# Performance work log

Measured on AMD Instinct MI355X. Metric: run time of the kernel, lower is better.

## Reference

```python
import jax, jax.numpy as jnp
import numpy as np

D_TOK = 1222
N_BOU = 80

def _pe(n, d):
    pos = np.arange(n, dtype=np.float32)[:, None]
    div = np.exp(np.arange(0, d, 2, dtype=np.float32) * (-np.log(10000.0) / d))
    pe = np.zeros((n, d), np.float32)
    pe[:, 0::2] = np.sin(pos * div)
    pe[:, 1::2] = np.cos(pos * div)
    return jnp.asarray(pe)

def _ln(x, g, b, eps=1e-5):
    m = jnp.mean(x, -1, keepdims=True)
    v = jnp.mean((x - m) ** 2, -1, keepdims=True)
    return (x - m) / jnp.sqrt(v + eps) * g + b

_gather = jax.vmap(lambda f, i: f[:, i[..., 0], i[..., 1]])  # f [C,H,W], i [...,2] -> [C,...]


def setup_inputs() -> dict:
    key = jax.random.key(0)
    ks = jax.random.split(key, 8)
    D, FF, N = D_TOK, 2048, N_BOU
    s = 0.02
    return {
        "curr_img_features": jax.random.normal(ks[0], (2, 1024, 224, 224), jnp.float32),
        "previous_boundary": jax.random.randint(ks[1], (2, N, 2), 0, 224, dtype=jnp.int32),
        "ln_g": jnp.ones((D,), jnp.float32), "ln_b": jnp.zeros((D,), jnp.float32),
        "in_proj_w": s * jax.random.normal(ks[2], (3 * D, D), jnp.float32),
        "in_proj_b": jnp.zeros((3 * D,), jnp.float32),
        "out_proj_w": s * jax.random.normal(ks[3], (D, D), jnp.float32),
        "out_proj_b": jnp.zeros((D,), jnp.float32),
        "lin1_w": s * jax.random.normal(ks[4], (FF, D), jnp.float32),
        "lin1_b": jnp.zeros((FF,), jnp.float32),
        "lin2_w": s * jax.random.normal(ks[5], (D, FF), jnp.float32),
        "lin2_b": jnp.zeros((D,), jnp.float32),
        "norm1_g": jnp.ones((D,), jnp.float32), "norm1_b": jnp.zeros((D,), jnp.float32),
        "norm2_g": jnp.ones((D,), jnp.float32), "norm2_b": jnp.zeros((D,), jnp.float32),
        "fc_w": s * jax.random.normal(ks[6], (N, 1026, D), jnp.float32),
        "fc_b": jnp.zeros((N, 1026), jnp.float32),
    }


def reference(curr_img_features, previous_boundary, ln_g, ln_b, in_proj_w, in_proj_b,
              out_proj_w, out_proj_b, lin1_w, lin1_b, lin2_w, lin2_b,
              norm1_g, norm1_b, norm2_g, norm2_b, fc_w, fc_b):
    D = D_TOK
    offs = jnp.array([[dx, dy] for dx in range(-3, 4) for dy in range(-3, 4)], jnp.int32)  # [49,2]
    # multi-scale avg-pooled + zero-padded maps (hoisted out of the refine loop; identical math)
    padded = []
    for s in range(4):
        k = 2 ** s
        f = curr_img_features
        if k > 1:
            B, C, H, W = f.shape
            f = f.reshape(B, C, H // k, k, W // k, k).mean((3, 5))
        padded.append(jnp.pad(f, ((0, 0), (0, 0), (3, 3), (3, 3))))
    pe = _pe(N_BOU, D)
    boundary = previous_boundary.astype(jnp.int32)
    results = []
    for _ in range(6):
        qf = _gather(curr_img_features, boundary)  # [B,C,N]
        dots = []
        for s in range(4):
            bs = boundary // (2 ** s)
            idx = bs[:, :, None, :] + offs[None, None] + 3  # [B,N,49,2] into padded map
            keyf = _gather(padded[s], idx)  # [B,C,N,49]
            dots.append(jnp.einsum('bcn,bcno->bno', qf, keyf))
        dots = jnp.concatenate(dots, axis=2)  # [B,N,196]
        tokens = jnp.concatenate([qf.transpose(0, 2, 1), dots,
                                  boundary.astype(jnp.float32)], axis=2)  # [B,N,1222]
        tokens = _ln(tokens, ln_g, ln_b)
        tokens = tokens + pe[None]  # positional encoding (dropout = eval/identity)
        # TransformerEncoderLayer, nhead=1, post-norm, relu, no dropout (eval)
        qkv = tokens @ in_proj_w.T + in_proj_b
        q, k_, v = jnp.split(qkv, 3, axis=-1)
        sc = jnp.einsum('bnd,bmd->bnm', q, k_) / jnp.sqrt(jnp.float32(D))
        attn = jax.nn.softmax(sc, axis=-1) @ v
        attn = attn @ out_proj_w.T + out_proj_b
        x = _ln(tokens + attn, norm1_g, norm1_b)
        ff = jax.nn.relu(x @ lin1_w.T + lin1_b) @ lin2_w.T + lin2_b
        x = _ln(x + ff, norm2_g, norm2_b)
        # 80 independent per-token heads, batched
        out = jnp.einsum('bnd,nod->bno', x, fc_w) + fc_b[None]  # [B,80,1026]
        off_f = out[..., :2]
        # torch .long() truncates toward zero; clip keeps gathers in-range (original clamp was a no-op bug)
        boundary = jnp.clip(boundary + jnp.trunc(off_f).astype(jnp.int32), 0, 223)
        results.append(boundary)
    return jnp.stack(results)  # [6,B,80,2] int32
```

## Files before the change

### kernel.cpp

```cpp
#include <hip/hip_runtime.h>
#include <math.h>

#define DTOK 1222
#define NBOU 80
#define MM   160
#define FFD  2048
#define OQKV 3666

typedef __attribute__((ext_vector_type(8))) short short8;
typedef __attribute__((ext_vector_type(4))) float f32x4;

__device__ __forceinline__ unsigned short f2bf(float x) {
  unsigned int u = __float_as_uint(x);
  unsigned int r = (u + 0x7FFFu + ((u >> 16) & 1u)) >> 16;
  return (unsigned short)r;
}
__device__ __forceinline__ float bf2f(unsigned short h) {
  return __uint_as_float((unsigned int)h << 16);
}

__device__ __forceinline__ float wave_red_sum(float v) {
#pragma unroll
  for (int off = 32; off; off >>= 1) v += __shfl_xor(v, off, 64);
  return v;
}
__device__ __forceinline__ float block_red_sum(float v, float* rb, int tid) {
  v = wave_red_sum(v);
  __syncthreads();
  if ((tid & 63) == 0) rb[tid >> 6] = v;
  __syncthreads();
  return rb[0] + rb[1] + rb[2] + rb[3];
}

__device__ __forceinline__ void frag_write_row(const float* __restrict__ row,
                                               short* __restrict__ Af,
                                               int r, int T, int tid) {
  int mt = r >> 6, mf = (r >> 4) & 3, rl = r & 15;
  for (int task = tid; task < T * 4; task += 256) {
    int t = task >> 2, kq = task & 3;
    const float* src = row + t * 32 + kq * 8;
    short8 h, l, q;
#pragma unroll
    for (int j = 0; j < 8; ++j) {
      float x = src[j];
      unsigned short hb = f2bf(x);
      float r1 = x - bf2f(hb);
      unsigned short lb = f2bf(r1);
      float r2 = r1 - bf2f(lb);
      h[j] = (short)hb; l[j] = (short)lb; q[j] = (short)f2bf(r2);
    }
    size_t base = (size_t)(mt * T + t) * 6144 + mf * 512 + (size_t)(rl + kq * 16) * 8;
    *(short8*)(Af + base) = h;
    *(short8*)(Af + base + 2048) = l;
    *(short8*)(Af + base + 4096) = q;
  }
}

__global__ __launch_bounds__(256) void k_nhwc0p(const float* __restrict__ f,
                                                float* __restrict__ L0n,
                                                float* __restrict__ L1) {
  int xt = blockIdx.x;
  int y1 = blockIdx.y;
  int zc = blockIdx.z;
  int b = zc >> 4, ct = zc & 15;
  __shared__ float tile[64][65];
  int tid = threadIdx.x;
  const float* fb = f + (size_t)b * 1024 * 50176;
#pragma unroll
  for (int i = 0; i < 16; ++i) {
    int u = tid + 256 * i;
    int xl = u & 31, r = (u >> 5) & 1, c = u >> 6;
    tile[c][xl + 32 * r] = fb[(size_t)(ct * 64 + c) * 50176 +
                              (size_t)(2 * y1 + r) * 224 + xt * 32 + xl];
  }
  __syncthreads();
#pragma unroll
  for (int i = 0; i < 16; ++i) {
    int u = tid + 256 * i;
    int c2 = u & 63, x2 = (u >> 6) & 31, r2 = u >> 11;
    L0n[(((size_t)b * 224 + 2 * y1 + r2) * 224 + xt * 32 + x2) * 1024 + ct * 64 + c2] =
        tile[c2][x2 + 32 * r2];
  }
#pragma unroll
  for (int i = 0; i < 4; ++i) {
    int u = tid + 256 * i;
    int c3 = u & 63, xp = u >> 6;
    float v = 0.25f * (tile[c3][2 * xp] + tile[c3][2 * xp + 1] +
                       tile[c3][32 + 2 * xp] + tile[c3][32 + 2 * xp + 1]);
    L1[(((size_t)b * 112 + y1) * 112 + xt * 16 + xp) * 1024 + ct * 64 + c3] = v;
  }
}

__global__ __launch_bounds__(256) void k_pool23(const float* __restrict__ L1,
                                                float* __restrict__ L2,
                                                float* __restrict__ L3) {
  int x3 = blockIdx.x, y3 = blockIdx.y, b = blockIdx.z;
  int c = threadIdx.x * 4;
  float4 l2v[2][2];
#pragma unroll
  for (int yy = 0; yy < 2; ++yy)
#pragma unroll
    for (int xx = 0; xx < 2; ++xx) {
      const float* p00 = L1 + (((size_t)(b * 112 + 4 * y3 + 2 * yy) * 112) + 4 * x3 + 2 * xx) * 1024 + c;
      const float* p01 = p00 + 1024;
      const float* p10 = p00 + (size_t)112 * 1024;
      const float* p11 = p10 + 1024;
      float4 a = *(const float4*)p00, bv = *(const float4*)p01;
      float4 cv = *(const float4*)p10, dv = *(const float4*)p11;
      float4 r;
      r.x = 0.25f * (a.x + bv.x + cv.x + dv.x);
      r.y = 0.25f * (a.y + bv.y + cv.y + dv.y);
      r.z = 0.25f * (a.z + bv.z + cv.z + dv.z);
      r.w = 0.25f * (a.w + bv.w + cv.w + dv.w);
      l2v[yy][xx] = r;
      *(float4*)(L2 + (((size_t)(b * 56 + 2 * y3 + yy) * 56) + 2 * x3 + xx) * 1024 + c) = r;
    }
  float4 r3;
  r3.x = 0.25f * (l2v[0][0].x + l2v[0][1].x + l2v[1][0].x + l2v[1][1].x);
  r3.y = 0.25f * (l2v[0][0].y + l2v[0][1].y + l2v[1][0].y + l2v[1][1].y);
  r3.z = 0.25f * (l2v[0][0].z + l2v[0][1].z + l2v[1][0].z + l2v[1][1].z);
  r3.w = 0.25f * (l2v[0][0].w + l2v[0][1].w + l2v[1][0].w + l2v[1][1].w);
  *(float4*)(L3 + (((size_t)(b * 28 + y3) * 28) + x3) * 1024 + c) = r3;
}

__global__ __launch_bounds__(256) void k_pe(float* __restrict__ pe, int* __restrict__ bnd,
                                            const int* __restrict__ pb) {
  int n = blockIdx.x, tid = threadIdx.x;
  for (int d = tid; d < DTOK; d += 256) {
    int i = d >> 1;
    double e = exp((double)(2 * i) * (-log(10000.0) / (double)DTOK));
    double ang = (double)n * e;
    pe[n * DTOK + d] = (float)((d & 1) ? cos(ang) : sin(ang));
  }
  if (n == 0) {
    for (int t = tid; t < 2 * NBOU * 2; t += 256) bnd[t] = pb[t];
  }
}

__global__ __launch_bounds__(256) void k_conv(const float* __restrict__ X,
                                              short* __restrict__ F,
                                              int R, int K, int T) {
  int b = blockIdx.x;
  int rt = b / T, t = b % T;
  int tid = threadIdx.x, mf = tid >> 6, lane = tid & 63;
  int row = rt * 64 + mf * 16 + (lane & 15);
  int k0 = t * 32 + (lane >> 4) * 8;
  float a[8];
#pragma unroll
  for (int j = 0; j < 8; ++j) {
    int k = k0 + j;
    a[j] = (row < R && k < K) ? X[(size_t)row * K + k] : 0.f;
  }
  short8 h, l, q;
#pragma unroll
  for (int j = 0; j < 8; ++j) {
    float x = a[j];
    unsigned short hb = f2bf(x);
    float r1 = x - bf2f(hb);
    unsigned short lb = f2bf(r1);
    float r2 = r1 - bf2f(lb);
    h[j] = (short)hb; l[j] = (short)lb; q[j] = (short)f2bf(r2);
  }
  size_t base = (size_t)b * 6144 + mf * 512 + (size_t)lane * 8;
  *(short8*)(F + base) = h;
  *(short8*)(F + base + 2048) = l;
  *(short8*)(F + base + 4096) = q;
}

__global__ __launch_bounds__(256) void k_dots(const float* __restrict__ L0n,
                                              const float* __restrict__ L1,
                                              const float* __restrict__ L2,
                                              const float* __restrict__ L3,
                                              const int* __restrict__ bnd,
                                              float* __restrict__ dots) {
  int o = blockIdx.x;
  int blk = blockIdx.y;
  int b = blk / NBOU;
  int tid = threadIdx.x, s = tid >> 6, lane = tid & 63;
  int bd0 = bnd[blk * 2 + 0], bd1 = bnd[blk * 2 + 1];
  const float* cp = L0n + (((size_t)b * 224 + bd0) * 224 + bd1) * 1024;
  int Hs = 224 >> s;
  const float* base = (s == 0) ? L0n : (s == 1) ? L1 : (s == 2) ? L2 : L3;
  int yy = (bd0 >> s) + o / 7 - 3;
  int xx = (bd1 >> s) + o % 7 - 3;
  float a = 0.f;
  if (yy >= 0 && yy < Hs && xx >= 0 && xx < Hs) {
    const float* kp = base + (((size_t)b * Hs + yy) * Hs + xx) * 1024;
#pragma unroll
    for (int j = 0; j < 4; ++j) {
      int c = (lane + 64 * j) * 4;
      float4 kv = *(const float4*)(kp + c);
      float4 qv = *(const float4*)(cp + c);
      a += kv.x * qv.x + kv.y * qv.y + kv.z * qv.z + kv.w * qv.w;
    }
  }
  a = wave_red_sum(a);
  if (lane == 0) dots[blk * 196 + s * 49 + o] = a;
}

__global__ __launch_bounds__(256) void k_tokln(const float* __restrict__ L0n,
                                               const int* __restrict__ bnd,
                                               const float* __restrict__ dots,
                                               const float* __restrict__ g,
                                               const float* __restrict__ bb,
                                               const float* __restrict__ pe,
                                               float* __restrict__ tok_out,
                                               short* __restrict__ Af, int T) {
  int blk = blockIdx.x;
  int b = blk / NBOU, n = blk % NBOU;
  int tid = threadIdx.x;
  __shared__ __align__(16) float token[1248];
  __shared__ float rbuf[8];
  int bd0 = bnd[blk * 2 + 0], bd1 = bnd[blk * 2 + 1];
  const float* cp = L0n + (((size_t)b * 224 + bd0) * 224 + bd1) * 1024;
  {
    int d = tid * 4;
    *(float4*)&token[d] = *(const float4*)(cp + d);
  }
  if (tid < 196) token[1024 + tid] = dots[blk * 196 + tid];
  if (tid == 0) { token[1220] = (float)bd0; token[1221] = (float)bd1; }
  if (tid < 26) token[1222 + tid] = 0.f;
  __syncthreads();

  float ls = 0.f;
  for (int d = tid; d < DTOK; d += 256) ls += token[d];
  float mean = block_red_sum(ls, rbuf, tid) * (1.0f / DTOK);
  float lq = 0.f;
  for (int d = tid; d < DTOK; d += 256) { float t = token[d] - mean; lq += t * t; }
  float var = block_red_sum(lq, rbuf, tid) * (1.0f / DTOK);
  float rstd = rsqrtf(var + 1e-5f);
  for (int d = tid; d < DTOK; d += 256) {
    float o = (token[d] - mean) * rstd * g[d] + bb[d] + pe[n * DTOK + d];
    tok_out[(size_t)blk * DTOK + d] = o;
    token[d] = o;
  }
  __syncthreads();
  frag_write_row(token, Af, blk, T, tid);
}

__global__ __launch_bounds__(256) void k_mfma2(const short* __restrict__ Af,
                                               const short* __restrict__ Bf,
                                               float* __restrict__ partial,
                                               int T, int O, int S) {
  int nt = blockIdx.x, sp = blockIdx.y;
  int tid = threadIdx.x, w = tid >> 6, lane = tid & 63;
  int wr = w >> 1, wc = w & 1;
  int rl = lane & 15, kq = lane >> 4;
  int cps = (T + S - 1) / S;
  int t0 = sp * cps, t1 = min(t0 + cps, T);

  f32x4 acc[3][2][2];
#pragma unroll
  for (int mt = 0; mt < 3; ++mt)
#pragma unroll
    for (int mi = 0; mi < 2; ++mi)
#pragma unroll
      for (int ni = 0; ni < 2; ++ni) acc[mt][mi][ni] = (f32x4){0.f, 0.f, 0.f, 0.f};

  const size_t bbase = (size_t)(wc * 2) * 512 + (size_t)lane * 8;
  const size_t abase = (size_t)(wr * 2) * 512 + (size_t)lane * 8;

  short8 bv[3][2], bv2[3][2];

#define LOADB(tt, BV)                                                          \
  {                                                                            \
    const short* bp = Bf + ((size_t)nt * T + (tt)) * 6144 + bbase;             \
    _Pragma("unroll")                                                          \
    for (int s = 0; s < 3; ++s)                                                \
      _Pragma("unroll")                                                        \
      for (int ni = 0; ni < 2; ++ni)                                           \
        BV[s][ni] = *(const short8*)(bp + s * 2048 + ni * 512);                \
  }

  if (t0 < t1) {
    LOADB(t0, bv);
    for (int t = t0; t < t1; ++t) {
      if (t + 1 < t1) LOADB(t + 1, bv2);
#pragma unroll
      for (int mt = 0; mt < 3; ++mt) {
        const short* ap = Af + ((size_t)(mt * T + t)) * 6144 + abase;
        short8 af[3][2];
#pragma unroll
        for (int s = 0; s < 3; ++s)
#pragma unroll
          for (int mi = 0; mi < 2; ++mi)
            af[s][mi] = *(const short8*)(ap + s * 2048 + mi * 512);
#pragma unroll
        for (int mi = 0; mi < 2; ++mi)
#pragma unroll
          for (int ni = 0; ni < 2; ++ni) {
            f32x4 a = acc[mt][mi][ni];
            a = __builtin_amdgcn_mfma_f32_16x16x32_bf16(af[0][mi], bv[0][ni], a, 0, 0, 0);
            a = __builtin_amdgcn_mfma_f32_16x16x32_bf16(af[0][mi], bv[1][ni], a, 0, 0, 0);
            a = __builtin_amdgcn_mfma_f32_16x16x32_bf16(af[1][mi], bv[0][ni], a, 0, 0, 0);
            a = __builtin_amdgcn_mfma_f32_16x16x32_bf16(af[0][mi], bv[2][ni], a, 0, 0, 0);
            a = __builtin_amdgcn_mfma_f32_16x16x32_bf16(af[2][mi], bv[0][ni], a, 0, 0, 0);
            a = __builtin_amdgcn_mfma_f32_16x16x32_bf16(af[1][mi], bv[1][ni], a, 0, 0, 0);
            acc[mt][mi][ni] = a;
          }
      }
#pragma unroll
      for (int s = 0; s < 3; ++s)
#pragma unroll
        for (int ni = 0; ni < 2; ++ni) bv[s][ni] = bv2[s][ni];
    }
  }
#undef LOADB

  float* pp = partial + (size_t)sp * MM * O;
#pragma unroll
  for (int mt = 0; mt < 3; ++mt)
#pragma unroll
    for (int mi = 0; mi < 2; ++mi)
#pragma unroll
      for (int ni = 0; ni < 2; ++ni) {
        int c = nt * 64 + wc * 32 + ni * 16 + rl;
        if (c >= O) continue;
#pragma unroll
        for (int reg = 0; reg < 4; ++reg) {
          int r = mt * 64 + wr * 32 + mi * 16 + kq * 4 + reg;
          if (r < MM) pp[(size_t)r * O + c] = acc[mt][mi][ni][reg];
        }
      }
}

__global__ __launch_bounds__(256) void k_red4(const float* __restrict__ partial,
                                              const float* __restrict__ bias,
                                              float* __restrict__ out,
                                              int O, int S) {
  size_t idx = ((size_t)blockIdx.x * 256 + threadIdx.x) * 4;
  size_t total = (size_t)MM * O;
  if (idx >= total) return;
  float4 v = *(const float4*)(partial + idx);
  for (int s = 1; s < S; ++s) {
    float4 p = *(const float4*)(partial + (size_t)s * total + idx);
    v.x += p.x; v.y += p.y; v.z += p.z; v.w += p.w;
  }
  float r[4] = {v.x, v.y, v.z, v.w};
#pragma unroll
  for (int j = 0; j < 4; ++j) r[j] += bias[(int)((idx + j) % O)];
  float4 wv = {r[0], r[1], r[2], r[3]};
  *(float4*)(out + idx) = wv;
}

__global__ __launch_bounds__(256) void k_redf(const float* __restrict__ partial,
                                              const float* __restrict__ bias,
                                              short* __restrict__ Af,
                                              int S, int T) {
  const int O = FFD;
  size_t idx8 = ((size_t)blockIdx.x * 256 + threadIdx.x) * 8;
  size_t total = (size_t)MM * O;
  if (idx8 >= total) return;
  int r = (int)(idx8 / O), c = (int)(idx8 % O);
  float v[8];
#pragma unroll
  for (int j = 0; j < 8; ++j) v[j] = 0.f;
  for (int s = 0; s < S; ++s) {
    const float* p = partial + (size_t)s * total + idx8;
#pragma unroll
    for (int j = 0; j < 8; ++j) v[j] += p[j];
  }
  short8 h, l, q;
#pragma unroll
  for (int j = 0; j < 8; ++j) {
    float x = fmaxf(v[j] + bias[c + j], 0.f);
    unsigned short hb = f2bf(x);
    float r1 = x - bf2f(hb);
    unsigned short lb = f2bf(r1);
    float r2 = r1 - bf2f(lb);
    h[j] = (short)hb; l[j] = (short)lb; q[j] = (short)f2bf(r2);
  }
  int mt = r >> 6, mf = (r >> 4) & 3, rl = r & 15;
  int t = c >> 5, kq = (c >> 3) & 3;
  size_t base = (size_t)(mt * T + t) * 6144 + mf * 512 + (size_t)(rl + kq * 16) * 8;
  *(short8*)(Af + base) = h;
  *(short8*)(Af + base + 2048) = l;
  *(short8*)(Af + base + 4096) = q;
}

__global__ __launch_bounds__(256) void k_redln(const float* __restrict__ partial,
                                               const float* __restrict__ bias,
                                               const float* __restrict__ res,
                                               const float* __restrict__ g,
                                               const float* __restrict__ bb,
                                               float* __restrict__ xout,
                                               short* __restrict__ Af,
                                               int S, int T) {
  const int O = DTOK;
  int m = blockIdx.x, tid = threadIdx.x;
  __shared__ __align__(16) float row[1248];
  __shared__ float rb[8];
  if (tid < 26) row[1222 + tid] = 0.f;
  float ls = 0.f;
  for (int d = tid; d < O; d += 256) {
    float v = 0.f;
    for (int s = 0; s < S; ++s) v += partial[((size_t)s * MM + m) * O + d];
    v += bias[d];
    v += res[(size_t)m * O + d];
    row[d] = v; ls += v;
  }
  float mean = block_red_sum(ls, rb, tid) * (1.0f / DTOK);
  float lq = 0.f;
  for (int d = tid; d < O; d += 256) { float t = row[d] - mean; lq += t * t; }
  float var = block_red_sum(lq, rb, tid) * (1.0f / DTOK);
  float rstd = rsqrtf(var + 1e-5f);
  for (int d = tid; d < O; d += 256) {
    float xn = (row[d] - mean) * rstd * g[d] + bb[d];
    xout[(size_t)m * O + d] = xn;
    row[d] = xn;
  }
  __syncthreads();
  frag_write_row(row, Af, m, T, tid);
}

__global__ __launch_bounds__(256) void k_redlnfc(const float* __restrict__ partial,
                                                 const float* __restrict__ bias,
                                                 const float* __restrict__ res,
                                                 const float* __restrict__ g,
                                                 const float* __restrict__ bb,
                                                 const float* __restrict__ fcw,
                                                 const float* __restrict__ fcb,
                                                 int* __restrict__ bnd,
                                                 int* __restrict__ outp,
                                                 int S) {
  const int O = DTOK;
  int blk = blockIdx.x;
  int n = blk % NBOU;
  int tid = threadIdx.x;
  __shared__ float row[DTOK];
  __shared__ float rb[8];
  float ls = 0.f;
  for (int d = tid; d < O; d += 256) {
    float v = 0.f;
    for (int s = 0; s < S; ++s) v += partial[((size_t)s * MM + blk) * O + d];
    v += bias[d];
    v += res[(size_t)blk * O + d];
    row[d] = v; ls += v;
  }
  float mean = block_red_sum(ls, rb, tid) * (1.0f / DTOK);
  float lq = 0.f;
  for (int d = tid; d < O; d += 256) { float t = row[d] - mean; lq += t * t; }
  float var = block_red_sum(lq, rb, tid) * (1.0f / DTOK);
  float rstd = rsqrtf(var + 1e-5f);
  const float* w0 = fcw + (size_t)n * 1026 * DTOK;
  const float* w1 = w0 + DTOK;
  float s0 = 0.f, s1 = 0.f;
  for (int d = tid; d < O; d += 256) {
    float xn = (row[d] - mean) * rstd * g[d] + bb[d];
    s0 += xn * w0[d];
    s1 += xn * w1[d];
  }
  s0 = block_red_sum(s0, rb, tid);
  s1 = block_red_sum(s1, rb, tid);
  if (tid == 0) {
    float o0 = s0 + fcb[n * 1026 + 0];
    float o1 = s1 + fcb[n * 1026 + 1];
    int b0 = bnd[blk * 2 + 0], b1 = bnd[blk * 2 + 1];
    int nb0 = b0 + (int)truncf(o0);
    int nb1 = b1 + (int)truncf(o1);
    nb0 = nb0 < 0 ? 0 : (nb0 > 223 ? 223 : nb0);
    nb1 = nb1 < 0 ? 0 : (nb1 > 223 ? 223 : nb1);
    bnd[blk * 2 + 0] = nb0;
    bnd[blk * 2 + 1] = nb1;
    outp[blk * 2 + 0] = nb0;
    outp[blk * 2 + 1] = nb1;
  }
}

__global__ __launch_bounds__(512) void k_attn3(const float* __restrict__ qkv,
                                               short* __restrict__ Af, int T) {
  int blk = blockIdx.x;
  int b = blk / NBOU;
  int tid = threadIdx.x, w = tid >> 6, lane = tid & 63;
  __shared__ __align__(16) float q[1224];
  __shared__ float sc[80];
  __shared__ __align__(16) float pv[8][1248];
  const float* qrow = qkv + (size_t)blk * OQKV;
  for (int d = tid; d < DTOK; d += 512) q[d] = qrow[d];
  __syncthreads();

#pragma unroll
  for (int i = 0; i < 10; ++i) {
    int m2 = w * 10 + i;
    const float* krow = qkv + (size_t)(b * NBOU + m2) * OQKV + DTOK;
    float a = 0.f;
#pragma unroll
    for (int j = 0; j < 20; ++j) {
      int d = lane + 64 * j;
      if (d < DTOK) a += q[d] * krow[d];
    }
    a = wave_red_sum(a);
    if (lane == 0) sc[m2] = a * (1.0f / 34.957116f);
  }
  __syncthreads();
  if (w == 0) {
    float x0 = sc[lane];
    float x1 = (lane < 16) ? sc[64 + lane] : -INFINITY;
    float mx = fmaxf(x0, x1);
#pragma unroll
    for (int off = 32; off; off >>= 1) mx = fmaxf(mx, __shfl_xor(mx, off, 64));
    float e0 = expf(x0 - mx);
    float e1 = (lane < 16) ? expf(x1 - mx) : 0.f;
    float ssum = wave_red_sum(e0 + e1);
    sc[lane] = e0 / ssum;
    if (lane < 16) sc[64 + lane] = e1 / ssum;
  }
  __syncthreads();

  float acc[20];
#pragma unroll
  for (int j = 0; j < 20; ++j) acc[j] = 0.f;
  for (int i = 0; i < 10; ++i) {
    int m2 = w * 10 + i;
    float pm = sc[m2];
    const float* vrow = qkv + (size_t)(b * NBOU + m2) * OQKV + 2 * DTOK;
#pragma unroll
    for (int j = 0; j < 20; ++j) {
      int d = lane + 64 * j;
      if (d < DTOK) acc[j] += pm * vrow[d];
    }
  }
#pragma unroll
  for (int j = 0; j < 20; ++j) {
    int d = lane + 64 * j;
    if (d < DTOK) pv[w][d] = acc[j];
  }
  __syncthreads();
  for (int d = tid; d < DTOK; d += 512) {
    float v = pv[0][d];
#pragma unroll
    for (int s = 1; s < 8; ++s) v += pv[s][d];
    pv[0][d] = v;
  }
  if (tid < 26) pv[0][1222 + tid] = 0.f;
  __syncthreads();
  frag_write_row(pv[0], Af, blk, T, tid);
}

extern "C" void kernel_launch(void* const* d_in, const int* in_sizes, int n_in,
                              void* d_out, int out_size, void* d_ws, size_t ws_size,
                              hipStream_t stream) {
  const float* f   = (const float*)d_in[0];
  const int*   pb  = (const int*)d_in[1];
  const float* lng = (const float*)d_in[2];
  const float* lnb = (const float*)d_in[3];
  const float* ipw = (const float*)d_in[4];
  const float* ipb = (const float*)d_in[5];
  const float* opw = (const float*)d_in[6];
  const float* opb = (const float*)d_in[7];
  const float* l1w = (const float*)d_in[8];
  const float* l1b = (const float*)d_in[9];
  const float* l2w = (const float*)d_in[10];
  const float* l2b = (const float*)d_in[11];
  const float* n1g = (const float*)d_in[12];
  const float* n1b = (const float*)d_in[13];
  const float* n2g = (const float*)d_in[14];
  const float* n2b = (const float*)d_in[15];
  const float* fcw = (const float*)d_in[16];
  const float* fcb = (const float*)d_in[17];
  int* outp = (int*)d_out;

  const int T1 = 39;
  const int T2 = 64;
  const int NT_IP = 58, NT_OP = 20, NT_L1 = 32, NT_L2 = 20;
  const int S_IP = 6, S_OP = 10, S_L1 = 8, S_L2 = 16;

  char* wsb = (char*)d_ws;
  auto alloc = [&](size_t bytes) -> char* {
    char* p = wsb;
    wsb += (bytes + 255) & ~(size_t)255;
    return p;
  };
  float* L0n  = (float*)alloc((size_t)2 * 224 * 224 * 1024 * 4);
  float* L1   = (float*)alloc((size_t)2 * 112 * 112 * 1024 * 4);
  float* L2   = (float*)alloc((size_t)2 * 56 * 56 * 1024 * 4);
  float* L3   = (float*)alloc((size_t)2 * 28 * 28 * 1024 * 4);
  float* pe   = (float*)alloc((size_t)NBOU * DTOK * 4);
  int*   bnd  = (int*)alloc(320 * 4);
  float* tokens = (float*)alloc((size_t)MM * DTOK * 4);
  float* qkvb   = (float*)alloc((size_t)MM * OQKV * 4);
  float* x1     = (float*)alloc((size_t)MM * DTOK * 4);
  float* dots   = (float*)alloc((size_t)MM * 196 * 4);
  short* Af1  = (short*)alloc((size_t)3 * T1 * 6144 * 2);
  short* Af2  = (short*)alloc((size_t)3 * T2 * 6144 * 2);
  short* ipWf = (short*)alloc((size_t)NT_IP * T1 * 6144 * 2);
  short* opWf = (short*)alloc((size_t)NT_OP * T1 * 6144 * 2);
  short* l1Wf = (short*)alloc((size_t)NT_L1 * T1 * 6144 * 2);
  short* l2Wf = (short*)alloc((size_t)NT_L2 * T2 * 6144 * 2);
  float* part = (float*)alloc((size_t)S_IP * MM * OQKV * 4);

  k_nhwc0p<<<dim3(7, 112, 32), 256, 0, stream>>>(f, L0n, L1);
  k_pool23<<<dim3(28, 28, 2), 256, 0, stream>>>(L1, L2, L3);
  k_pe<<<NBOU, 256, 0, stream>>>(pe, bnd, pb);

  k_conv<<<NT_IP * T1, 256, 0, stream>>>(ipw, ipWf, OQKV, DTOK, T1);
  k_conv<<<NT_OP * T1, 256, 0, stream>>>(opw, opWf, DTOK, DTOK, T1);
  k_conv<<<NT_L1 * T1, 256, 0, stream>>>(l1w, l1Wf, FFD, DTOK, T1);
  k_conv<<<NT_L2 * T2, 256, 0, stream>>>(l2w, l2Wf, DTOK, FFD, T2);

  for (int it = 0; it < 6; ++it) {
    k_dots<<<dim3(49, 160), 256, 0, stream>>>(L0n, L1, L2, L3, bnd, dots);
    k_tokln<<<160, 256, 0, stream>>>(L0n, bnd, dots, lng, lnb, pe, tokens, Af1, T1);

    k_mfma2<<<dim3(NT_IP, S_IP), 256, 0, stream>>>(Af1, ipWf, part, T1, OQKV, S_IP);
    k_red4<<<(MM * OQKV + 1023) / 1024, 256, 0, stream>>>(part, ipb, qkvb, OQKV, S_IP);

    k_attn3<<<160, 512, 0, stream>>>(qkvb, Af1, T1);

    k_mfma2<<<dim3(NT_OP, S_OP), 256, 0, stream>>>(Af1, opWf, part, T1, DTOK, S_OP);
    k_redln<<<160, 256, 0, stream>>>(part, opb, tokens, n1g, n1b, x1, Af1, S_OP, T1);

    k_mfma2<<<dim3(NT_L1, S_L1), 256, 0, stream>>>(Af1, l1Wf, part, T1, FFD, S_L1);
    k_redf<<<MM * FFD / 2048, 256, 0, stream>>>(part, l1b, Af2, S_L1, T2);

    k_mfma2<<<dim3(NT_L2, S_L2), 256, 0, stream>>>(Af2, l2Wf, part, T2, DTOK, S_L2);
    k_redlnfc<<<160, 256, 0, stream>>>(part, l2b, x1, n2g, n2b, fcw, fcb, bnd, outp + it * 320, S_L2);
  }
}
```

Measured before the change: 1.269 ms.

## Fuse refine-loop kernels into one persistent cooperative kernel with grid syncs

Replaces the 66 per-iteration kernel launches (dots, token LN, four split-K GEMMs, reductions, attention, LN/fc head) with a single cooperative persistent kernel. It loops over the phases with grid-wide barriers and grid-stride task loops, and falls back to separate launches if the cooperative launch fails. Attention is also rewritten to run with 256 threads (4 waves) instead of 512. The aim is to remove launch overhead and inter-kernel gaps in a latency-bound loop. The cost is grid.sync overhead, fewer resident blocks (2 per CU under launch bounds), and some phases running with less parallelism than before.

New measurement: 4.037 ms. +218.2%, slower.

```diff
diff --git a/kernel.cpp b/kernel.cpp
--- a/kernel.cpp
+++ b/kernel.cpp
@@ -1,11 +1,25 @@
 #include <hip/hip_runtime.h>
+#include <hip/hip_cooperative_groups.h>
 #include <math.h>
+
+namespace cg = cooperative_groups;
 
 #define DTOK 1222
 #define NBOU 80
 #define MM   160
 #define FFD  2048
 #define OQKV 3666
+
+#define T1c 39
+#define T2c 64
+#define NT_IPc 58
+#define NT_OPc 20
+#define NT_L1c 32
+#define NT_L2c 20
+#define S_IPc 6
+#define S_OPc 10
+#define S_L1c 8
+#define S_L2c 16
 
 typedef __attribute__((ext_vector_type(8))) short short8;
 typedef __attribute__((ext_vector_type(4))) float f32x4;
@@ -59,9 +73,7 @@
 __global__ __launch_bounds__(256) void k_nhwc0p(const float* __restrict__ f,
                                                 float* __restrict__ L0n,
                                                 float* __restrict__ L1) {
-  int xt = blockIdx.x;
-  int y1 = blockIdx.y;
-  int zc = blockIdx.z;
+  int xt = blockIdx.x, y1 = blockIdx.y, zc = blockIdx.z;
   int b = zc >> 4, ct = zc & 15;
   __shared__ float tile[64][65];
   int tid = threadIdx.x;
@@ -167,374 +179,412 @@
   *(short8*)(F + base + 4096) = q;
 }
 
-__global__ __launch_bounds__(256) void k_dots(const float* __restrict__ L0n,
-                                              const float* __restrict__ L1,
-                                              const float* __restrict__ L2,
-                                              const float* __restrict__ L3,
-                                              const int* __restrict__ bnd,
-                                              float* __restrict__ dots) {
-  int o = blockIdx.x;
-  int blk = blockIdx.y;
-  int b = blk / NBOU;
-  int tid = threadIdx.x, s = tid >> 6, lane = tid & 63;
-  int bd0 = bnd[blk * 2 + 0], bd1 = bnd[blk * 2 + 1];
-  const float* cp = L0n + (((size_t)b * 224 + bd0) * 224 + bd1) * 1024;
-  int Hs = 224 >> s;
-  const float* base = (s == 0) ? L0n : (s == 1) ? L1 : (s == 2) ? L2 : L3;
-  int yy = (bd0 >> s) + o / 7 - 3;
-  int xx = (bd1 >> s) + o % 7 - 3;
-  float a = 0.f;
-  if (yy >= 0 && yy < Hs && xx >= 0 && xx < Hs) {
-    const float* kp = base + (((size_t)b * Hs + yy) * Hs + xx) * 1024;
-#pragma unroll
-    for (int j = 0; j < 4; ++j) {
-      int c = (lane + 64 * j) * 4;
-      float4 kv = *(const float4*)(kp + c);
-      float4 qv = *(const float4*)(cp + c);
-      a += kv.x * qv.x + kv.y * qv.y + kv.z * qv.z + kv.w * qv.w;
-    }
-  }
-  a = wave_red_sum(a);
-  if (lane == 0) dots[blk * 196 + s * 49 + o] = a;
-}
-
-__global__ __launch_bounds__(256) void k_tokln(const float* __restrict__ L0n,
-                                               const int* __restrict__ bnd,
-                                               const float* __restrict__ dots,
-                                               const float* __restrict__ g,
-                                               const float* __restrict__ bb,
-                                               const float* __restrict__ pe,
-                                               float* __restrict__ tok_out,
-                                               short* __restrict__ Af, int T) {
-  int blk = blockIdx.x;
-  int b = blk / NBOU, n = blk % NBOU;
+struct Params {
+  const float *L0n, *L1, *L2, *L3;
+  const float *lng, *lnb, *pe;
+  const float *ipb, *opb, *l1b, *l2b;
+  const float *n1g, *n1b, *n2g, *n2b;
+  const float *fcw, *fcb;
+  const short *ipWf, *opWf, *l1Wf, *l2Wf;
+  short *Af1, *Af2;
+  float *tokens, *qkvb, *x1, *dots, *part;
+  int *bnd, *outp;
+};
+
+__device__ __forceinline__ void ph_dots(const Params& p, int tid) {
+  int s = tid >> 6, lane = tid & 63;
+  for (int task = blockIdx.x; task < 49 * 160; task += gridDim.x) {
+    int o = task % 49, blk = task / 49;
+    int b = blk / NBOU;
+    int bd0 = p.bnd[blk * 2 + 0], bd1 = p.bnd[blk * 2 + 1];
+    const float* cp = p.L0n + (((size_t)b * 224 + bd0) * 224 + bd1) * 1024;
+    int Hs = 224 >> s;
+    const float* base = (s == 0) ? p.L0n : (s == 1) ? p.L1 : (s == 2) ? p.L2 : p.L3;
+    int yy = (bd0 >> s) + o / 7 - 3;
+    int xx = (bd1 >> s) + o % 7 - 3;
+    float a = 0.f;
+    if (yy >= 0 && yy < Hs && xx >= 0 && xx < Hs) {
+      const float* kp = base + (((size_t)b * Hs + yy) * Hs + xx) * 1024;
+#pragma unroll
+      for (int j = 0; j < 4; ++j) {
+        int c = (lane + 64 * j) * 4;
+        float4 kv = *(const float4*)(kp + c);
+        float4 qv = *(const float4*)(cp + c);
+        a += kv.x * qv.x + kv.y * qv.y + kv.z * qv.z + kv.w * qv.w;
+      }
+    }
+    a = wave_red_sum(a);
+    if (lane == 0) p.dots[blk * 196 + s * 49 + o] = a;
+  }
+}
+
+__device__ __forceinline__ void ph_tokln(const Params& p, int tid,
+                                         float* token, float* rbuf) {
+  for (int blk = blockIdx.x; blk < 160; blk += gridDim.x) {
+    int b = blk / NBOU, n = blk % NBOU;
+    int bd0 = p.bnd[blk * 2 + 0], bd1 = p.bnd[blk * 2 + 1];
+    const float* cp = p.L0n + (((size_t)b * 224 + bd0) * 224 + bd1) * 1024;
+    {
+      int d = tid * 4;
+      *(float4*)&token[d] = *(const float4*)(cp + d);
+    }
+    if (tid < 196) token[1024 + tid] = p.dots[blk * 196 + tid];
+    if (tid == 0) { token[1220] = (float)bd0; token[1221] = (float)bd1; }
+    if (tid < 26) token[1222 + tid] = 0.f;
+    __syncthreads();
+    float ls = 0.f;
+    for (int d = tid; d < DTOK; d += 256) ls += token[d];
+    float mean = block_red_sum(ls, rbuf, tid) * (1.0f / DTOK);
+    float lq = 0.f;
+    for (int d = tid; d < DTOK; d += 256) { float t = token[d] - mean; lq += t * t; }
+    float var = block_red_sum(lq, rbuf, tid) * (1.0f / DTOK);
+    float rstd = rsqrtf(var + 1e-5f);
+    for (int d = tid; d < DTOK; d += 256) {
+      float o = (token[d] - mean) * rstd * p.lng[d] + p.lnb[d] + p.pe[n * DTOK + d];
+      p.tokens[(size_t)blk * DTOK + d] = o;
+      token[d] = o;
+    }
+    __syncthreads();
+    frag_write_row(token, p.Af1, blk, T1c, tid);
+    __syncthreads();
+  }
+}
+
+__device__ __forceinline__ void ph_gemm(const short* __restrict__ Af,
+                                        const short* __restrict__ Bf,
+                                        float* __restrict__ partial,
+                                        int T, int O, int S, int NT, int tid) {
+  int w = tid >> 6, lane = tid & 63;
+  int wr = w >> 1, wc = w & 1;
+  int rl = lane & 15, kq = lane >> 4;
+  const size_t bbase = (size_t)(wc * 2) * 512 + (size_t)lane * 8;
+  const size_t abase = (size_t)(wr * 2) * 512 + (size_t)lane * 8;
+  for (int task = blockIdx.x; task < NT * S; task += gridDim.x) {
+    int nt = task % NT, sp = task / NT;
+    int cps = (T + S - 1) / S;
+    int t0 = sp * cps, t1 = min(t0 + cps, T);
+    f32x4 acc[3][2][2];
+#pragma unroll
+    for (int mt = 0; mt < 3; ++mt)
+#pragma unroll
+      for (int mi = 0; mi < 2; ++mi)
+#pragma unroll
+        for (int ni = 0; ni < 2; ++ni) acc[mt][mi][ni] = (f32x4){0.f, 0.f, 0.f, 0.f};
+    short8 bv[3][2], bv2[3][2];
+#define LOADB(tt, BV)                                                          \
+    {                                                                          \
+      const short* bp = Bf + ((size_t)nt * T + (tt)) * 6144 + bbase;           \
+      _Pragma("unroll")                                                        \
+      for (int s = 0; s < 3; ++s)                                              \
+        _Pragma("unroll")                                                      \
+        for (int ni = 0; ni < 2; ++ni)                                         \
+          BV[s][ni] = *(const short8*)(bp + s * 2048 + ni * 512);              \
+    }
+    if (t0 < t1) {
+      LOADB(t0, bv);
+      for (int t = t0; t < t1; ++t) {
+        if (t + 1 < t1) LOADB(t + 1, bv2);
+#pragma unroll
+        for (int mt = 0; mt < 3; ++mt) {
+          const short* ap = Af + ((size_t)(mt * T + t)) * 6144 + abase;
+          short8 af[3][2];
+#pragma unroll
+          for (int s = 0; s < 3; ++s)
+#pragma unroll
+            for (int mi = 0; mi < 2; ++mi)
+              af[s][mi] = *(const short8*)(ap + s * 2048 + mi * 512);
+#pragma unroll
+          for (int mi = 0; mi < 2; ++mi)
+#pragma unroll
+            for (int ni = 0; ni < 2; ++ni) {
+              f32x4 a = acc[mt][mi][ni];
+              a = __builtin_amdgcn_mfma_f32_16x16x32_bf16(af[0][mi], bv[0][ni], a, 0, 0, 0);
+              a = __builtin_amdgcn_mfma_f32_16x16x32_bf16(af[0][mi], bv[1][ni], a, 0, 0, 0);
+              a = __builtin_amdgcn_mfma_f32_16x16x32_bf16(af[1][mi], bv[0][ni], a, 0, 0, 0);
+              a = __builtin_amdgcn_mfma_f32_16x16x32_bf16(af[0][mi], bv[2][ni], a, 0, 0, 0);
+              a = __builtin_amdgcn_mfma_f32_16x16x32_bf16(af[2][mi], bv[0][ni], a, 0, 0, 0);
+              a = __builtin_amdgcn_mfma_f32_16x16x32_bf16(af[1][mi], bv[1][ni], a, 0, 0, 0);
+              acc[mt][mi][ni] = a;
+            }
+        }
+#pragma unroll
+        for (int s = 0; s < 3; ++s)
+#pragma unroll
+          for (int ni = 0; ni < 2; ++ni) bv[s][ni] = bv2[s][ni];
+      }
+    }
+#undef LOADB
+    float* pp = partial + (size_t)sp * MM * O;
+#pragma unroll
+    for (int mt = 0; mt < 3; ++mt)
+#pragma unroll
+      for (int mi = 0; mi < 2; ++mi)
+#pragma unroll
+        for (int ni = 0; ni < 2; ++ni) {
+          int c = nt * 64 + wc * 32 + ni * 16 + rl;
+          if (c >= O) continue;
+#pragma unroll
+          for (int reg = 0; reg < 4; ++reg) {
+            int r = mt * 64 + wr * 32 + mi * 16 + kq * 4 + reg;
+            if (r < MM) pp[(size_t)r * O + c] = acc[mt][mi][ni][reg];
+          }
+        }
+  }
+}
+
+__device__ __forceinline__ void ph_red4(const Params& p, int tid) {
+  const int O = OQKV, S = S_IPc;
+  size_t total = (size_t)MM * O;
+  size_t stride = (size_t)gridDim.x * 256 * 4;
+  for (size_t idx = ((size_t)blockIdx.x * 256 + tid) * 4; idx < total; idx += stride) {
+    float4 v = *(const float4*)(p.part + idx);
+    for (int s = 1; s < S; ++s) {
+      float4 q = *(const float4*)(p.part + (size_t)s * total + idx);
+      v.x += q.x; v.y += q.y; v.z += q.z; v.w += q.w;
+    }
+    float r[4] = {v.x, v.y, v.z, v.w};
+#pragma unroll
+    for (int j = 0; j < 4; ++j) r[j] += p.ipb[(int)((idx + j) % O)];
+    float4 wv = {r[0], r[1], r[2], r[3]};
+    *(float4*)(p.qkvb + idx) = wv;
+  }
+}
+
+__device__ __forceinline__ void ph_attn(const Params& p, int tid,
+                                        float (*pv)[1248], float* sc) {
+  int wave = tid >> 6, lane = tid & 63;
+  for (int blk = blockIdx.x; blk < 160; blk += gridDim.x) {
+    int b = blk / NBOU;
+    float qr[20];
+    const float* qrow = p.qkvb + (size_t)blk * OQKV;
+#pragma unroll
+    for (int j = 0; j < 20; ++j) {
+      int d = lane + 64 * j;
+      qr[j] = (d < DTOK) ? qrow[d] : 0.f;
+    }
+    for (int i = 0; i < 20; ++i) {
+      int m2 = wave * 20 + i;
+      const float* krow = p.qkvb + (size_t)(b * NBOU + m2) * OQKV + DTOK;
+      float a = 0.f;
+#pragma unroll
+      for (int j = 0; j < 20; ++j) {
+        int d = lane + 64 * j;
+        if (d < DTOK) a += qr[j] * krow[d];
+      }
+      a = wave_red_sum(a);
+      if (lane == 0) sc[m2] = a * (1.0f / 34.957116f);
+    }
+    __syncthreads();
+    if (wave == 0) {
+      float x0 = sc[lane];
+      float x1 = (lane < 16) ? sc[64 + lane] : -INFINITY;
+      float mx = fmaxf(x0, x1);
+#pragma unroll
+      for (int off = 32; off; off >>= 1) mx = fmaxf(mx, __shfl_xor(mx, off, 64));
+      float e0 = expf(x0 - mx);
+      float e1 = (lane < 16) ? expf(x1 - mx) : 0.f;
+      float ssum = wave_red_sum(e0 + e1);
+      sc[lane] = e0 / ssum;
+      if (lane < 16) sc[64 + lane] = e1 / ssum;
+    }
+    __syncthreads();
+    float acc[20];
+#pragma unroll
+    for (int j = 0; j < 20; ++j) acc[j] = 0.f;
+    for (int i = 0; i < 20; ++i) {
+      int m2 = wave * 20 + i;
+      float pm = sc[m2];
+      const float* vrow = p.qkvb + (size_t)(b * NBOU + m2) * OQKV + 2 * DTOK;
+#pragma unroll
+      for (int j = 0; j < 20; ++j) {
+        int d = lane + 64 * j;
+        if (d < DTOK) acc[j] += pm * vrow[d];
+      }
+    }
+#pragma unroll
+    for (int j = 0; j < 20; ++j) {
+      int d = lane + 64 * j;
+      if (d < DTOK) pv[wave][d] = acc[j];
+    }
+    __syncthreads();
+    for (int d = tid; d < DTOK; d += 256)
+      pv[0][d] = ((pv[0][d] + pv[1][d]) + pv[2][d]) + pv[3][d];
+    if (tid < 26) pv[0][1222 + tid] = 0.f;
+    __syncthreads();
+    frag_write_row(pv[0], p.Af1, blk, T1c, tid);
+    __syncthreads();
+  }
+}
+
+__device__ __forceinline__ void ph_redln(const Params& p, int tid,
+                                         float* row, float* rb) {
+  const int O = DTOK, S = S_OPc;
+  for (int m = blockIdx.x; m < 160; m += gridDim.x) {
+    if (tid < 26) row[1222 + tid] = 0.f;
+    float ls = 0.f;
+    for (int d = tid; d < O; d += 256) {
+      float v = 0.f;
+      for (int s = 0; s < S; ++s) v += p.part[((size_t)s * MM + m) * O + d];
+      v += p.opb[d];
+      v += p.tokens[(size_t)m * O + d];
+      row[d] = v; ls += v;
+    }
+    float mean = block_red_sum(ls, rb, tid) * (1.0f / DTOK);
+    float lq = 0.f;
+    for (int d = tid; d < O; d += 256) { float t = row[d] - mean; lq += t * t; }
+    float var = block_red_sum(lq, rb, tid) * (1.0f / DTOK);
+    float rstd = rsqrtf(var + 1e-5f);
+    for (int d = tid; d < O; d += 256) {
+      float xn = (row[d] - mean) * rstd * p.n1g[d] + p.n1b[d];
+      p.x1[(size_t)m * O + d] = xn;
+      row[d] = xn;
+    }
+    __syncthreads();
+    frag_write_row(row, p.Af1, m, T1c, tid);
+    __syncthreads();
+  }
+}
+
+__device__ __forceinline__ void ph_redf(const Params& p, int tid) {
+  const int O = FFD, S = S_L1c, T = T2c;
+  size_t total = (size_t)MM * O;
+  size_t stride = (size_t)gridDim.x * 256 * 8;
+  for (size_t idx8 = ((size_t)blockIdx.x * 256 + tid) * 8; idx8 < total; idx8 += stride) {
+    int r = (int)(idx8 / O), c = (int)(idx8 % O);
+    float v[8];
+#pragma unroll
+    for (int j = 0; j < 8; ++j) v[j] = 0.f;
+    for (int s = 0; s < S; ++s) {
+      const float* q = p.part + (size_t)s * total + idx8;
+#pragma unroll
+      for (int j = 0; j < 8; ++j) v[j] += q[j];
+    }
+    short8 h, l, q8;
+#pragma unroll
+    for (int j = 0; j < 8; ++j) {
+      float x = fmaxf(v[j] + p.l1b[c + j], 0.f);
+      unsigned short hb = f2bf(x);
+      float r1 = x - bf2f(hb);
+      unsigned short lb = f2bf(r1);
+      float r2 = r1 - bf2f(lb);
+      h[j] = (short)hb; l[j] = (short)lb; q8[j] = (short)f2bf(r2);
+    }
+    int mt = r >> 6, mf = (r >> 4) & 3, rl = r & 15;
+    int t = c >> 5, kq = (c >> 3) & 3;
+    size_t base = (size_t)(mt * T + t) * 6144 + mf * 512 + (size_t)(rl + kq * 16) * 8;
+    *(short8*)(p.Af2 + base) = h;
+    *(short8*)(p.Af2 + base + 2048) = l;
+    *(short8*)(p.Af2 + base + 4096) = q8;
+  }
+}
+
+__device__ __forceinline__ void ph_redlnfc(const Params& p, int tid, int it,
+                                           float* row, float* rb) {
+  const int O = DTOK, S = S_L2c;
+  for (int blk = blockIdx.x; blk < 160; blk += gridDim.x) {
+    int n = blk % NBOU;
+    float ls = 0.f;
+    for (int d = tid; d < O; d += 256) {
+      float v = 0.f;
+      for (int s = 0; s < S; ++s) v += p.part[((size_t)s * MM + blk) * O + d];
+      v += p.l2b[d];
+      v += p.x1[(size_t)blk * O + d];
+      row[d] = v; ls += v;
+    }
+    float mean = block_red_sum(ls, rb, tid) * (1.0f / DTOK);
+    float lq = 0.f;
+    for (int d = tid; d < O; d += 256) { float t = row[d] - mean; lq += t * t; }
+    float var = block_red_sum(lq, rb, tid) * (1.0f / DTOK);
+    float rstd = rsqrtf(var + 1e-5f);
+    const float* w0 = p.fcw + (size_t)n * 1026 * DTOK;
+    const float* w1 = w0 + DTOK;
+    float s0 = 0.f, s1 = 0.f;
+    for (int d = tid; d < O; d += 256) {
+      float xn = (row[d] - mean) * rstd * p.n2g[d] + p.n2b[d];
+      s0 += xn * w0[d];
+      s1 += xn * w1[d];
+    }
+    s0 = block_red_sum(s0, rb, tid);
+    s1 = block_red_sum(s1, rb, tid);
+    if (tid == 0) {
+      float o0 = s0 + p.fcb[n * 1026 + 0];
+      float o1 = s1 + p.fcb[n * 1026 + 1];
+      int b0 = p.bnd[blk * 2 + 0], b1 = p.bnd[blk * 2 + 1];
+      int nb0 = b0 + (int)truncf(o0);
+      int nb1 = b1 + (int)truncf(o1);
+      nb0 = nb0 < 0 ? 0 : (nb0 > 223 ? 223 : nb0);
+      nb1 = nb1 < 0 ? 0 : (nb1 > 223 ? 223 : nb1);
+      p.bnd[blk * 2 + 0] = nb0;
+      p.bnd[blk * 2 + 1] = nb1;
+      p.outp[it * 320 + blk * 2 + 0] = nb0;
+      p.outp[it * 320 + blk * 2 + 1] = nb1;
+    }
+    __syncthreads();
+  }
+}
+
+__global__ __launch_bounds__(256, 2) void k_mega(Params p) {
+  cg::grid_group grid = cg::this_grid();
+  __shared__ __align__(16) float smem4[4][1248];
+  __shared__ float aux[96];
   int tid = threadIdx.x;
+  for (int it = 0; it < 6; ++it) {
+    ph_dots(p, tid);
+    grid.sync();
+    ph_tokln(p, tid, smem4[0], aux + 80);
+    grid.sync();
+    ph_gemm(p.Af1, p.ipWf, p.part, T1c, OQKV, S_IPc, NT_IPc, tid);
+    grid.sync();
+    ph_red4(p, tid);
+    grid.sync();
+    ph_attn(p, tid, smem4, aux);
+    grid.sync();
+    ph_gemm(p.Af1, p.opWf, p.part, T1c, DTOK, S_OPc, NT_OPc, tid);
+    grid.sync();
+    ph_redln(p, tid, smem4[0], aux + 80);
+    grid.sync();
+    ph_gemm(p.Af1, p.l1Wf, p.part, T1c, FFD, S_L1c, NT_L1c, tid);
+    grid.sync();
+    ph_redf(p, tid);
+    grid.sync();
+    ph_gemm(p.Af2, p.l2Wf, p.part, T2c, DTOK, S_L2c, NT_L2c, tid);
+    grid.sync();
+    ph_redlnfc(p, tid, it, smem4[0], aux + 80);
+    grid.sync();
+  }
+}
+
+__global__ __launch_bounds__(256) void kw_dots(Params p) { ph_dots(p, threadIdx.x); }
+__global__ __launch_bounds__(256) void kw_tokln(Params p) {
   __shared__ __align__(16) float token[1248];
   __shared__ float rbuf[8];
-  int bd0 = bnd[blk * 2 + 0], bd1 = bnd[blk * 2 + 1];
-  const float* cp = L0n + (((size_t)b * 224 + bd0) * 224 + bd1) * 1024;
-  {
-    int d = tid * 4;
-    *(float4*)&token[d] = *(const float4*)(cp + d);
-  }
-  if (tid < 196) token[1024 + tid] = dots[blk * 196 + tid];
-  if (tid == 0) { token[1220] = (float)bd0; token[1221] = (float)bd1; }
-  if (tid < 26) token[1222 + tid] = 0.f;
-  __syncthreads();
-
-  float ls = 0.f;
-  for (int d = tid; d < DTOK; d += 256) ls += token[d];
-  float mean = block_red_sum(ls, rbuf, tid) * (1.0f / DTOK);
-  float lq = 0.f;
-  for (int d = tid; d < DTOK; d += 256) { float t = token[d] - mean; lq += t * t; }
-  float var = block_red_sum(lq, rbuf, tid) * (1.0f / DTOK);
-  float rstd = rsqrtf(var + 1e-5f);
-  for (int d = tid; d < DTOK; d += 256) {
-    float o = (token[d] - mean) * rstd * g[d] + bb[d] + pe[n * DTOK + d];
-    tok_out[(size_t)blk * DTOK + d] = o;
-    token[d] = o;
-  }
-  __syncthreads();
-  frag_write_row(token, Af, blk, T, tid);
-}
-
-__global__ __launch_bounds__(256) void k_mfma2(const short* __restrict__ Af,
-                                               const short* __restrict__ Bf,
-                                               float* __restrict__ partial,
-                                               int T, int O, int S) {
-  int nt = blockIdx.x, sp = blockIdx.y;
-  int tid = threadIdx.x, w = tid >> 6, lane = tid & 63;
-  int wr = w >> 1, wc = w & 1;
-  int rl = lane & 15, kq = lane >> 4;
-  int cps = (T + S - 1) / S;
-  int t0 = sp * cps, t1 = min(t0 + cps, T);
-
-  f32x4 acc[3][2][2];
-#pragma unroll
-  for (int mt = 0; mt < 3; ++mt)
-#pragma unroll
-    for (int mi = 0; mi < 2; ++mi)
-#pragma unroll
-      for (int ni = 0; ni < 2; ++ni) acc[mt][mi][ni] = (f32x4){0.f, 0.f, 0.f, 0.f};
-
-  const size_t bbase = (size_t)(wc * 2) * 512 + (size_t)lane * 8;
-  const size_t abase = (size_t)(wr * 2) * 512 + (size_t)lane * 8;
-
-  short8 bv[3][2], bv2[3][2];
-
-#define LOADB(tt, BV)                                                          \
-  {                                                                            \
-    const short* bp = Bf + ((size_t)nt * T + (tt)) * 6144 + bbase;             \
-    _Pragma("unroll")                                                          \
-    for (int s = 0; s < 3; ++s)                                                \
-      _Pragma("unroll")                                                        \
-      for (int ni = 0; ni < 2; ++ni)                                           \
-        BV[s][ni] = *(const short8*)(bp + s * 2048 + ni * 512);                \
-  }
-
-  if (t0 < t1) {
-    LOADB(t0, bv);
-    for (int t = t0; t < t1; ++t) {
-      if (t + 1 < t1) LOADB(t + 1, bv2);
-#pragma unroll
-      for (int mt = 0; mt < 3; ++mt) {
-        const short* ap = Af + ((size_t)(mt * T + t)) * 6144 + abase;
-        short8 af[3][2];
-#pragma unroll
-        for (int s = 0; s < 3; ++s)
-#pragma unroll
-          for (int mi = 0; mi < 2; ++mi)
-            af[s][mi] = *(const short8*)(ap + s * 2048 + mi * 512);
-#pragma unroll
-        for (int mi = 0; mi < 2; ++mi)
-#pragma unroll
-          for (int ni = 0; ni < 2; ++ni) {
-            f32x4 a = acc[mt][mi][ni];
-            a = __builtin_amdgcn_mfma_f32_16x16x32_bf16(af[0][mi], bv[0][ni], a, 0, 0, 0);
-            a = __builtin_amdgcn_mfma_f32_16x16x32_bf16(af[0][mi], bv[1][ni], a, 0, 0, 0);
-            a = __builtin_amdgcn_mfma_f32_16x16x32_bf16(af[1][mi], bv[0][ni], a, 0, 0, 0);
-            a = __builtin_amdgcn_mfma_f32_16x16x32_bf16(af[0][mi], bv[2][ni], a, 0, 0, 0);
-            a = __builtin_amdgcn_mfma_f32_16x16x32_bf16(af[2][mi], bv[0][ni], a, 0, 0, 0);
-            a = __builtin_amdgcn_mfma_f32_16x16x32_bf16(af[1][mi], bv[1][ni], a, 0, 0, 0);
-            acc[mt][mi][ni] = a;
-          }
-      }
-#pragma unroll
-      for (int s = 0; s < 3; ++s)
-#pragma unroll
-        for (int ni = 0; ni < 2; ++ni) bv[s][ni] = bv2[s][ni];
-    }
-  }
-#undef LOADB
-
-  float* pp = partial + (size_t)sp * MM * O;
-#pragma unroll
-  for (int mt = 0; mt < 3; ++mt)
-#pragma unroll
-    for (int mi = 0; mi < 2; ++mi)
-#pragma unroll
-      for (int ni = 0; ni < 2; ++ni) {
-        int c = nt * 64 + wc * 32 + ni * 16 + rl;
-        if (c >= O) continue;
-#pragma unroll
-        for (int reg = 0; reg < 4; ++reg) {
-          int r = mt * 64 + wr * 32 + mi * 16 + kq * 4 + reg;
-          if (r < MM) pp[(size_t)r * O + c] = acc[mt][mi][ni][reg];
-        }
-      }
-}
-
-__global__ __launch_bounds__(256) void k_red4(const float* __restrict__ partial,
-                                              const float* __restrict__ bias,
-                                              float* __restrict__ out,
-                                              int O, int S) {
-  size_t idx = ((size_t)blockIdx.x * 256 + threadIdx.x) * 4;
-  size_t total = (size_t)MM * O;
-  if (idx >= total) return;
-  float4 v = *(const float4*)(partial + idx);
-  for (int s = 1; s < S; ++s) {
-    float4 p = *(const float4*)(partial + (size_t)s * total + idx);
-    v.x += p.x; v.y += p.y; v.z += p.z; v.w += p.w;
-  }
-  float r[4] = {v.x, v.y, v.z, v.w};
-#pragma unroll
-  for (int j = 0; j < 4; ++j) r[j] += bias[(int)((idx + j) % O)];
-  float4 wv = {r[0], r[1], r[2], r[3]};
-  *(float4*)(out + idx) = wv;
-}
-
-__global__ __launch_bounds__(256) void k_redf(const float* __restrict__ partial,
-                                              const float* __restrict__ bias,
-                                              short* __restrict__ Af,
-                                              int S, int T) {
-  const int O = FFD;
-  size_t idx8 = ((size_t)blockIdx.x * 256 + threadIdx.x) * 8;
-  size_t total = (size_t)MM * O;
-  if (idx8 >= total) return;
-  int r = (int)(idx8 / O), c = (int)(idx8 % O);
-  float v[8];
-#pragma unroll
-  for (int j = 0; j < 8; ++j) v[j] = 0.f;
-  for (int s = 0; s < S; ++s) {
-    const float* p = partial + (size_t)s * total + idx8;
-#pragma unroll
-    for (int j = 0; j < 8; ++j) v[j] += p[j];
-  }
-  short8 h, l, q;
-#pragma unroll
-  for (int j = 0; j < 8; ++j) {
-    float x = fmaxf(v[j] + bias[c + j], 0.f);
-    unsigned short hb = f2bf(x);
-    float r1 = x - bf2f(hb);
-    unsigned short lb = f2bf(r1);
-    float r2 = r1 - bf2f(lb);
-    h[j] = (short)hb; l[j] = (short)lb; q[j] = (short)f2bf(r2);
-  }
-  int mt = r >> 6, mf = (r >> 4) & 3, rl = r & 15;
-  int t = c >> 5, kq = (c >> 3) & 3;
-  size_t base = (size_t)(mt * T + t) * 6144 + mf * 512 + (size_t)(rl + kq * 16) * 8;
-  *(short8*)(Af + base) = h;
-  *(short8*)(Af + base + 2048) = l;
-  *(short8*)(Af + base + 4096) = q;
-}
-
-__global__ __launch_bounds__(256) void k_redln(const float* __restrict__ partial,
-                                               const float* __restrict__ bias,
-                                               const float* __restrict__ res,
-                                               const float* __restrict__ g,
-                                               const float* __restrict__ bb,
-                                               float* __restrict__ xout,
-                                               short* __restrict__ Af,
-                                               int S, int T) {
-  const int O = DTOK;
-  int m = blockIdx.x, tid = threadIdx.x;
+  ph_tokln(p, threadIdx.x, token, rbuf);
+}
+__global__ __launch_bounds__(256) void kw_gemm(Params p, int which) {
+  const short* Af = (which == 3) ? p.Af2 : p.Af1;
+  const short* Bf = (which == 0) ? p.ipWf : (which == 1) ? p.opWf : (which == 2) ? p.l1Wf : p.l2Wf;
+  int T = (which == 3) ? T2c : T1c;
+  int O = (which == 0) ? OQKV : (which == 2) ? FFD : DTOK;
+  int S = (which == 0) ? S_IPc : (which == 1) ? S_OPc : (which == 2) ? S_L1c : S_L2c;
+  int NT = (which == 0) ? NT_IPc : (which == 1) ? NT_OPc : (which == 2) ? NT_L1c : NT_L2c;
+  ph_gemm(Af, Bf, p.part, T, O, S, NT, threadIdx.x);
+}
+__global__ __launch_bounds__(256) void kw_red4(Params p) { ph_red4(p, threadIdx.x); }
+__global__ __launch_bounds__(256) void kw_attn(Params p) {
+  __shared__ __align__(16) float pv[4][1248];
+  __shared__ float sc[80];
+  ph_attn(p, threadIdx.x, pv, sc);
+}
+__global__ __launch_bounds__(256) void kw_redln(Params p) {
   __shared__ __align__(16) float row[1248];
   __shared__ float rb[8];
-  if (tid < 26) row[1222 + tid] = 0.f;
-  float ls = 0.f;
-  for (int d = tid; d < O; d += 256) {
-    float v = 0.f;
-    for (int s = 0; s < S; ++s) v += partial[((size_t)s * MM + m) * O + d];
-    v += bias[d];
-    v += res[(size_t)m * O + d];
-    row[d] = v; ls += v;
-  }
-  float mean = block_red_sum(ls, rb, tid) * (1.0f / DTOK);
-  float lq = 0.f;
-  for (int d = tid; d < O; d += 256) { float t = row[d] - mean; lq += t * t; }
-  float var = block_red_sum(lq, rb, tid) * (1.0f / DTOK);
-  float rstd = rsqrtf(var + 1e-5f);
-  for (int d = tid; d < O; d += 256) {
-    float xn = (row[d] - mean) * rstd * g[d] + bb[d];
-    xout[(size_t)m * O + d] = xn;
-    row[d] = xn;
-  }
-  __syncthreads();
-  frag_write_row(row, Af, m, T, tid);
-}
-
-__global__ __launch_bounds__(256) void k_redlnfc(const float* __restrict__ partial,
-                                                 const float* __restrict__ bias,
-                                                 const float* __restrict__ res,
-                                                 const float* __restrict__ g,
-                                                 const float* __restrict__ bb,
-                                                 const float* __restrict__ fcw,
-                                                 const float* __restrict__ fcb,
-                                                 int* __restrict__ bnd,
-                                                 int* __restrict__ outp,
-                                                 int S) {
-  const int O = DTOK;
-  int blk = blockIdx.x;
-  int n = blk % NBOU;
-  int tid = threadIdx.x;
-  __shared__ float row[DTOK];
+  ph_redln(p, threadIdx.x, row, rb);
+}
+__global__ __launch_bounds__(256) void kw_redf(Params p) { ph_redf(p, threadIdx.x); }
+__global__ __launch_bounds__(256) void kw_redlnfc(Params p, int it) {
+  __shared__ __align__(16) float row[1248];
   __shared__ float rb[8];
-  float ls = 0.f;
-  for (int d = tid; d < O; d += 256) {
-    float v = 0.f;
-    for (int s = 0; s < S; ++s) v += partial[((size_t)s * MM + blk) * O + d];
-    v += bias[d];
-    v += res[(size_t)blk * O + d];
-    row[d] = v; ls += v;
-  }
-  float mean = block_red_sum(ls, rb, tid) * (1.0f / DTOK);
-  float lq = 0.f;
-  for (int d = tid; d < O; d += 256) { float t = row[d] - mean; lq += t * t; }
-  float var = block_red_sum(lq, rb, tid) * (1.0f / DTOK);
-  float rstd = rsqrtf(var + 1e-5f);
-  const float* w0 = fcw + (size_t)n * 1026 * DTOK;
-  const float* w1 = w0 + DTOK;
-  float s0 = 0.f, s1 = 0.f;
-  for (int d = tid; d < O; d += 256) {
-    float xn = (row[d] - mean) * rstd * g[d] + bb[d];
-    s0 += xn * w0[d];
-    s1 += xn * w1[d];
-  }
-  s0 = block_red_sum(s0, rb, tid);
-  s1 = block_red_sum(s1, rb, tid);
-  if (tid == 0) {
-    float o0 = s0 + fcb[n * 1026 + 0];
-    float o1 = s1 + fcb[n * 1026 + 1];
-    int b0 = bnd[blk * 2 + 0], b1 = bnd[blk * 2 + 1];
-    int nb0 = b0 + (int)truncf(o0);
-    int nb1 = b1 + (int)truncf(o1);
-    nb0 = nb0 < 0 ? 0 : (nb0 > 223 ? 223 : nb0);
-    nb1 = nb1 < 0 ? 0 : (nb1 > 223 ? 223 : nb1);
-    bnd[blk * 2 + 0] = nb0;
-    bnd[blk * 2 + 1] = nb1;
-    outp[blk * 2 + 0] = nb0;
-    outp[blk * 2 + 1] = nb1;
-  }
-}
-
-__global__ __launch_bounds__(512) void k_attn3(const float* __restrict__ qkv,
-                                               short* __restrict__ Af, int T) {
-  int blk = blockIdx.x;
-  int b = blk / NBOU;
-  int tid = threadIdx.x, w = tid >> 6, lane = tid & 63;
-  __shared__ __align__(16) float q[1224];
-  __shared__ float sc[80];
-  __shared__ __align__(16) float pv[8][1248];
-  const float* qrow = qkv + (size_t)blk * OQKV;
-  for (int d = tid; d < DTOK; d += 512) q[d] = qrow[d];
-  __syncthreads();
-
-#pragma unroll
-  for (int i = 0; i < 10; ++i) {
-    int m2 = w * 10 + i;
-    const float* krow = qkv + (size_t)(b * NBOU + m2) * OQKV + DTOK;
-    float a = 0.f;
-#pragma unroll
-    for (int j = 0; j < 20; ++j) {
-      int d = lane + 64 * j;
-      if (d < DTOK) a += q[d] * krow[d];
-    }
-    a = wave_red_sum(a);
-    if (lane == 0) sc[m2] = a * (1.0f / 34.957116f);
-  }
-  __syncthreads();
-  if (w == 0) {
-    float x0 = sc[lane];
-    float x1 = (lane < 16) ? sc[64 + lane] : -INFINITY;
-    float mx = fmaxf(x0, x1);
-#pragma unroll
-    for (int off = 32; off; off >>= 1) mx = fmaxf(mx, __shfl_xor(mx, off, 64));
-    float e0 = expf(x0 - mx);
-    float e1 = (lane < 16) ? expf(x1 - mx) : 0.f;
-    float ssum = wave_red_sum(e0 + e1);
-    sc[lane] = e0 / ssum;
-    if (lane < 16) sc[64 + lane] = e1 / ssum;
-  }
-  __syncthreads();
-
-  float acc[20];
-#pragma unroll
-  for (int j = 0; j < 20; ++j) acc[j] = 0.f;
-  for (int i = 0; i < 10; ++i) {
-    int m2 = w * 10 + i;
-    float pm = sc[m2];
-    const float* vrow = qkv + (size_t)(b * NBOU + m2) * OQKV + 2 * DTOK;
-#pragma unroll
-    for (int j = 0; j < 20; ++j) {
-      int d = lane + 64 * j;
-      if (d < DTOK) acc[j] += pm * vrow[d];
-    }
-  }
-#pragma unroll
-  for (int j = 0; j < 20; ++j) {
-    int d = lane + 64 * j;
-    if (d < DTOK) pv[w][d] = acc[j];
-  }
-  __syncthreads();
-  for (int d = tid; d < DTOK; d += 512) {
-    float v = pv[0][d];
-#pragma unroll
-    for (int s = 1; s < 8; ++s) v += pv[s][d];
-    pv[0][d] = v;
-  }
-  if (tid < 26) pv[0][1222 + tid] = 0.f;
-  __syncthreads();
-  frag_write_row(pv[0], Af, blk, T, tid);
+  ph_redlnfc(p, threadIdx.x, it, row, rb);
 }
 
 extern "C" void kernel_launch(void* const* d_in, const int* in_sizes, int n_in,
@@ -560,11 +610,6 @@
   const float* fcb = (const float*)d_in[17];
   int* outp = (int*)d_out;
 
-  const int T1 = 39;
-  const int T2 = 64;
-  const int NT_IP = 58, NT_OP = 20, NT_L1 = 32, NT_L2 = 20;
-  const int S_IP = 6, S_OP = 10, S_L1 = 8, S_L2 = 16;
-
   char* wsb = (char*)d_ws;
   auto alloc = [&](size_t bytes) -> char* {
     char* p = wsb;
@@ -581,39 +626,59 @@
   float* qkvb   = (float*)alloc((size_t)MM * OQKV * 4);
   float* x1     = (float*)alloc((size_t)MM * DTOK * 4);
   float* dots   = (float*)alloc((size_t)MM * 196 * 4);
-  short* Af1  = (short*)alloc((size_t)3 * T1 * 6144 * 2);
-  short* Af2  = (short*)alloc((size_t)3 * T2 * 6144 * 2);
-  short* ipWf = (short*)alloc((size_t)NT_IP * T1 * 6144 * 2);
-  short* opWf = (short*)alloc((size_t)NT_OP * T1 * 6144 * 2);
-  short* l1Wf = (short*)alloc((size_t)NT_L1 * T1 * 6144 * 2);
-  short* l2Wf = (short*)alloc((size_t)NT_L2 * T2 * 6144 * 2);
-  float* part = (float*)alloc((size_t)S_IP * MM * OQKV * 4);
+  short* Af1  = (short*)alloc((size_t)3 * T1c * 6144 * 2);
+  short* Af2  = (short*)alloc((size_t)3 * T2c * 6144 * 2);
+  short* ipWf = (short*)alloc((size_t)NT_IPc * T1c * 6144 * 2);
+  short* opWf = (short*)alloc((size_t)NT_OPc * T1c * 6144 * 2);
+  short* l1Wf = (short*)alloc((size_t)NT_L1c * T1c * 6144 * 2);
+  short* l2Wf = (short*)alloc((size_t)NT_L2c * T2c * 6144 * 2);
+  size_t partA = (size_t)S_L2c * MM * DTOK * 4;
+  size_t partB = (size_t)S_IPc * MM * OQKV * 4;
+  float* part = (float*)alloc(partA > partB ? partA : partB);
 
   k_nhwc0p<<<dim3(7, 112, 32), 256, 0, stream>>>(f, L0n, L1);
   k_pool23<<<dim3(28, 28, 2), 256, 0, stream>>>(L1, L2, L3);
   k_pe<<<NBOU, 256, 0, stream>>>(pe, bnd, pb);
 
-  k_conv<<<NT_IP * T1, 256, 0, stream>>>(ipw, ipWf, OQKV, DTOK, T1);
-  k_conv<<<NT_OP * T1, 256, 0, stream>>>(opw, opWf, DTOK, DTOK, T1);
-  k_conv<<<NT_L1 * T1, 256, 0, stream>>>(l1w, l1Wf, FFD, DTOK, T1);
-  k_conv<<<NT_L2 * T2, 256, 0, stream>>>(l2w, l2Wf, DTOK, FFD, T2);
-
-  for (int it = 0; it < 6; ++it) {
-    k_dots<<<dim3(49, 160), 256, 0, stream>>>(L0n, L1, L2, L3, bnd, dots);
-    k_tokln<<<160, 256, 0, stream>>>(L0n, bnd, dots, lng, lnb, pe, tokens, Af1, T1);
-
-    k_mfma2<<<dim3(NT_IP, S_IP), 256, 0, stream>>>(Af1, ipWf, part, T1, OQKV, S_IP);
-    k_red4<<<(MM * OQKV + 1023) / 1024, 256, 0, stream>>>(part, ipb, qkvb, OQKV, S_IP);
-
-    k_attn3<<<160, 512, 0, stream>>>(qkvb, Af1, T1);
-
-    k_mfma2<<<dim3(NT_OP, S_OP), 256, 0, stream>>>(Af1, opWf, part, T1, DTOK, S_OP);
-    k_redln<<<160, 256, 0, stream>>>(part, opb, tokens, n1g, n1b, x1, Af1, S_OP, T1);
-
-    k_mfma2<<<dim3(NT_L1, S_L1), 256, 0, stream>>>(Af1, l1Wf, part, T1, FFD, S_L1);
-    k_redf<<<MM * FFD / 2048, 256, 0, stream>>>(part, l1b, Af2, S_L1, T2);
-
-    k_mfma2<<<dim3(NT_L2, S_L2), 256, 0, stream>>>(Af2, l2Wf, part, T2, DTOK, S_L2);
-    k_redlnfc<<<160, 256, 0, stream>>>(part, l2b, x1, n2g, n2b, fcw, fcb, bnd, outp + it * 320, S_L2);
-  }
-}
+  k_conv<<<NT_IPc * T1c, 256, 0, stream>>>(ipw, ipWf, OQKV, DTOK, T1c);
+  k_conv<<<NT_OPc * T1c, 256, 0, stream>>>(opw, opWf, DTOK, DTOK, T1c);
+  k_conv<<<NT_L1c * T1c, 256, 0, stream>>>(l1w, l1Wf, FFD, DTOK, T1c);
+  k_conv<<<NT_L2c * T2c, 256, 0, stream>>>(l2w, l2Wf, DTOK, FFD, T2c);
+
+  Params prm;
+  prm.L0n = L0n; prm.L1 = L1; prm.L2 = L2; prm.L3 = L3;
+  prm.lng = lng; prm.lnb = lnb; prm.pe = pe;
+  prm.ipb = ipb; prm.opb = opb; prm.l1b = l1b; prm.l2b = l2b;
+  prm.n1g = n1g; prm.n1b = n1b; prm.n2g = n2g; prm.n2b = n2b;
+  prm.fcw = fcw; prm.fcb = fcb;
+  prm.ipWf = ipWf; prm.opWf = opWf; prm.l1Wf = l1Wf; prm.l2Wf = l2Wf;
+  prm.Af1 = Af1; prm.Af2 = Af2;
+  prm.tokens = tokens; prm.qkvb = qkvb; prm.x1 = x1; prm.dots = dots; prm.part = part;
+  prm.bnd = bnd; prm.outp = outp;
+
+  int maxBlocksPerCU = 0;
+  hipError_t occErr = hipOccupancyMaxActiveBlocksPerMultiprocessor(&maxBlocksPerCU, k_mega, 256, 0);
+  bool coopOK = false;
+  if (occErr == hipSuccess && maxBlocksPerCU >= 1) {
+    int bpc = maxBlocksPerCU < 2 ? maxBlocksPerCU : 2;
+    dim3 grid(bpc * 256);
+    void* args[] = {&prm};
+    hipError_t le = hipLaunchCooperativeKernel((const void*)k_mega, grid, dim3(256), args, 0, stream);
+    if (le == hipSuccess) coopOK = true;
+  }
+  if (!coopOK) {
+    for (int it = 0; it < 6; ++it) {
+      kw_dots<<<49 * 160, 256, 0, stream>>>(prm);
+      kw_tokln<<<160, 256, 0, stream>>>(prm);
+      kw_gemm<<<NT_IPc * S_IPc, 256, 0, stream>>>(prm, 0);
+      kw_red4<<<573, 256, 0, stream>>>(prm);
+      kw_attn<<<160, 256, 0, stream>>>(prm);
+      kw_gemm<<<NT_OPc * S_OPc, 256, 0, stream>>>(prm, 1);
+      kw_redln<<<160, 256, 0, stream>>>(prm);
+      kw_gemm<<<NT_L1c * S_L1c, 256, 0, stream>>>(prm, 2);
+      kw_redf<<<160, 256, 0, stream>>>(prm);
+      kw_gemm<<<NT_L2c * S_L2c, 256, 0, stream>>>(prm, 3);
+      kw_redlnfc<<<160, 256, 0, stream>>>(prm, it);
+    }
+  }
+}
```
